# Kernel tuning notes

Hardware: AMD Instinct MI355X
Metric: run time of the kernel (lower is better)

Reference implementation:

```python
import jax, jax.numpy as jnp
import numpy as np

B, S, D = 2, 2048, 1024
H, DK, DV = 16, 64, 64
DF = 4096
EPS = 1e-5


def _layer_norm(x, g, b):
    mu = jnp.mean(x, axis=-1, keepdims=True)
    var = jnp.mean((x - mu) ** 2, axis=-1, keepdims=True)
    return (x - mu) * jax.lax.rsqrt(var + EPS) * g + b


def setup_inputs() -> dict:
    key = jax.random.key(0)
    ks = jax.random.split(key, 12)
    s = lambda fan_in: 1.0 / np.sqrt(fan_in)
    return {
        "enc_input": jax.random.normal(ks[0], (B, S, D), dtype=jnp.float32),
        "wq": jax.random.uniform(ks[1], (D, H * DK), jnp.float32, -s(D), s(D)),
        "wk": jax.random.uniform(ks[2], (D, H * DK), jnp.float32, -s(D), s(D)),
        "wv": jax.random.uniform(ks[3], (D, H * DV), jnp.float32, -s(D), s(D)),
        "wo": jax.random.uniform(ks[4], (H * DV, D), jnp.float32, -s(H * DV), s(H * DV)),
        "w1": jax.random.uniform(ks[5], (D, DF), jnp.float32, -s(D), s(D)),
        "b1": jax.random.uniform(ks[6], (DF,), jnp.float32, -s(D), s(D)),
        "w2": jax.random.uniform(ks[7], (DF, D), jnp.float32, -s(DF), s(DF)),
        "b2": jax.random.uniform(ks[8], (D,), jnp.float32, -s(DF), s(DF)),
        "ln1_g": jnp.ones((D,), jnp.float32),
        "ln1_b": jnp.zeros((D,), jnp.float32),
        "ln2_g": jnp.ones((D,), jnp.float32),
        "ln2_b": jnp.zeros((D,), jnp.float32),
    }


def reference(enc_input, wq, wk, wv, wo, w1, b1, w2, b2, ln1_g, ln1_b, ln2_g, ln2_b):
    x = enc_input
    # QKV projections -> [B, H, S, d]
    q = (x @ wq).reshape(B, S, H, DK).transpose(0, 2, 1, 3)
    k = (x @ wk).reshape(B, S, H, DK).transpose(0, 2, 1, 3)
    v = (x @ wv).reshape(B, S, H, DV).transpose(0, 2, 1, 3)
    # scaled dot-product attention (scale = 1/sqrt(d_k), dropout is identity at eval)
    score = jnp.einsum("bhqd,bhkd->bhqk", q, k) / jnp.sqrt(jnp.float32(DK))
    attn = jax.nn.softmax(score, axis=-1)
    ctx = jnp.einsum("bhqk,bhkd->bhqd", attn, v)
    ctx = ctx.transpose(0, 2, 1, 3).reshape(B, S, H * DV)
    atn_out = ctx @ wo
    # Add & Norm 1
    h = _layer_norm(x + atn_out, ln1_g, ln1_b)
    # FFN
    ffn = jax.nn.relu(h @ w1 + b1) @ w2 + b2
    # Add & Norm 2
    return _layer_norm(h + ffn, ln2_g, ln2_b)
```

## Files before the change

kernel.cpp:

```cpp
#include <hip/hip_runtime.h>
#include <hip/hip_bf16.h>

typedef __bf16 bf16;
typedef __bf16 bf16x4 __attribute__((ext_vector_type(4)));
typedef __bf16 bf16x8 __attribute__((ext_vector_type(8)));
typedef float  f32x4  __attribute__((ext_vector_type(4)));

#define KB 2
#define KS 2048
#define KD 1024
#define KH 16
#define KM (KB*KS)
#define KQKVN 3072
#define KDF 4096

__device__ __forceinline__ f32x4 mfma16(bf16x8 a, bf16x8 b, f32x4 c) {
  return __builtin_amdgcn_mfma_f32_16x16x32_bf16(a, b, c, 0, 0, 0);
}

__device__ __forceinline__ float exp2_hw(float x) {
  float r;
  asm("v_exp_f32 %0, %1" : "=v"(r) : "v"(x));
  return r;
}

__device__ __forceinline__ void g2l16(const bf16* g, bf16* l) {
  __builtin_amdgcn_global_load_lds(
      (const __attribute__((address_space(1))) unsigned int*)g,
      (__attribute__((address_space(3))) unsigned int*)l, 16, 0, 0);
}

__global__ __launch_bounds__(256) void cvt_bf16_kernel(const float* __restrict__ in,
                                                       bf16* __restrict__ out, int n) {
  int i = (blockIdx.x * 256 + threadIdx.x) * 4;
  if (i >= n) return;
  f32x4 v = *reinterpret_cast<const f32x4*>(in + i);
  bf16x4 o;
  o[0] = (bf16)v[0]; o[1] = (bf16)v[1]; o[2] = (bf16)v[2]; o[3] = (bf16)v[3];
  *reinterpret_cast<bf16x4*>(out + i) = o;
}

struct WT4 { const float* src[4]; bf16* dst[4]; };

__global__ __launch_bounds__(256) void wtrans4_kernel(WT4 jobs) {
  __shared__ float tile[32][33];
  const float* W = jobs.src[blockIdx.z];
  bf16* WT = jobs.dst[blockIdx.z];
  const int n0 = blockIdx.x * 32, k0 = blockIdx.y * 32;
  const int tx = threadIdx.x & 31, ty = threadIdx.x >> 5;
#pragma unroll
  for (int j = ty; j < 32; j += 8) tile[j][tx] = W[(size_t)(k0 + j) * 1024 + n0 + tx];
  __syncthreads();
#pragma unroll
  for (int j = ty; j < 32; j += 8)
    WT[(size_t)(n0 + j) * 1024 + k0 + tx] = (bf16)tile[tx][j];
}

__global__ __launch_bounds__(256) void wtrans_big_kernel(const float* __restrict__ w1,
                                                         bf16* __restrict__ w1T,
                                                         const float* __restrict__ w2,
                                                         bf16* __restrict__ w2T) {
  __shared__ float tile[32][33];
  const float* W; bf16* WT; int K, N, n0, k0;
  if (blockIdx.z == 0) {
    W = w1; WT = w1T; K = 1024; N = 4096;
    n0 = blockIdx.x * 32; k0 = blockIdx.y * 32;
  } else {
    W = w2; WT = w2T; K = 4096; N = 1024;
    n0 = blockIdx.y * 32; k0 = blockIdx.x * 32;
  }
  const int tx = threadIdx.x & 31, ty = threadIdx.x >> 5;
#pragma unroll
  for (int j = ty; j < 32; j += 8) tile[j][tx] = W[(size_t)(k0 + j) * N + n0 + tx];
  __syncthreads();
#pragma unroll
  for (int j = ty; j < 32; j += 8) WT[(size_t)(n0 + j) * K + k0 + tx] = (bf16)tile[tx][j];
}

__global__ __launch_bounds__(256) void kvpack_kernel(const bf16* __restrict__ qkv,
                                                     bf16* __restrict__ kp,
                                                     bf16* __restrict__ vt) {
  __shared__ bf16 tile[64][72];
  const int s0 = blockIdx.x * 64;
  const int bh = blockIdx.y;
  const int b = bh >> 4, h = bh & 15;
  const int t = threadIdx.x;
  const int r = t >> 3, c8 = (t & 7) * 8;
#pragma unroll
  for (int rr = r; rr < 64; rr += 32) {
    const size_t grow = (size_t)(b * KS + s0 + rr) * KQKVN + h * 64 + c8;
    bf16x8 kv = *reinterpret_cast<const bf16x8*>(&qkv[grow + 1024]);
    *reinterpret_cast<bf16x8*>(&kp[((size_t)bh * KS + s0 + rr) * 64 + c8]) = kv;
    bf16x8 vv = *reinterpret_cast<const bf16x8*>(&qkv[grow + 2048]);
#pragma unroll
    for (int j = 0; j < 8; j++) tile[rr][c8 + j] = vv[j];
  }
  __syncthreads();
#pragma unroll
  for (int dd = r; dd < 64; dd += 32) {
    bf16x8 v;
#pragma unroll
    for (int j = 0; j < 8; j++) {
      const int pi = c8 + j;
      const int key = ((pi >> 5) << 5) | (((pi >> 2) & 1) << 4) |
                      (((pi >> 3) & 3) << 2) | (pi & 3);
      v[j] = tile[key][dd];
    }
    *reinterpret_cast<bf16x8*>(&vt[(size_t)bh * 64 * KS + (size_t)dd * KS + s0 + c8]) = v;
  }
}

struct P4 { bf16* p[4]; };

template <typename OUT_T, bool RELU, bool HAS_BIAS, bool SPLITK>
__global__ __launch_bounds__(512, 2) void gemm8p(const bf16* __restrict__ A,
                                                 const bf16* __restrict__ BT,
                                                 OUT_T* __restrict__ C, P4 pr,
                                                 const float* __restrict__ bias,
                                                 int M, int N, int K, int Kslice) {
  extern __shared__ __align__(16) bf16 sm[];
  const int tid = threadIdx.x, lane = tid & 63, w = tid >> 6;
  const int wr = w >> 2, wc = w & 3;
  const int gx = gridDim.x;
  const int nwg = gx * gridDim.y;
  int flat = blockIdx.y * gx + blockIdx.x;
  flat = (flat & 7) * (nwg >> 3) + (flat >> 3);
  const int bn = (flat % gx) * 256;
  const int bm = (flat / gx) * 256;
  const int z = blockIdx.z;
  const int NT = (SPLITK ? Kslice : K) >> 6;
  const int lr = lane & 15, hi = lane >> 4;
  const int sqrow = tid >> 3;
  const int sslot = tid & 7;
  const bf16* Abase = A + (size_t)bm * K + (SPLITK ? z * Kslice : 0);
  const bf16* Bbase = BT + (size_t)bn * K + (SPLITK ? z * Kslice : 0);
  auto stageQ = [&](int t, int p) {
    const int row = p * 64 + sqrow;
    const int col = (sslot ^ (row & 7)) * 8;
    bf16* dst = sm + (size_t)(t & 1) * 32768 + p * 4096 + w * 512;
    g2l16(Abase + (size_t)row * K + t * 64 + col, dst);
    g2l16(Bbase + (size_t)row * K + t * 64 + col, dst + 16384);
  };
  f32x4 acc[8][4] = {};
  stageQ(0, 0); stageQ(0, 1); stageQ(0, 2); stageQ(0, 3);
  for (int t = 0; t < NT; t++) {
    const char* sa = (const char*)(sm + (size_t)(t & 1) * 32768);
    const char* sb = sa + 32768;
    bf16x8 af[4], bfr[4];
    if (t + 1 < NT) {
      stageQ(t + 1, 0);
      stageQ(t + 1, 1);
      asm volatile("s_waitcnt vmcnt(4)" ::: "memory");
    } else {
      asm volatile("s_waitcnt vmcnt(0)" ::: "memory");
    }
    __builtin_amdgcn_sched_barrier(0);
    __builtin_amdgcn_s_barrier();
    __builtin_amdgcn_sched_barrier(0);
#pragma unroll
    for (int mfp = 0; mfp < 4; mfp++) {
      const int row = wr * 128 + mfp * 16 + lr;
      af[mfp] = *(const bf16x8*)(sa + row * 128 + ((hi ^ (row & 7)) * 16));
    }
#pragma unroll
    for (int nf = 0; nf < 4; nf++) {
      const int row = wc * 64 + nf * 16 + lr;
      bfr[nf] = *(const bf16x8*)(sb + row * 128 + ((hi ^ (row & 7)) * 16));
    }
    asm volatile("s_waitcnt lgkmcnt(0)" ::: "memory");
    __builtin_amdgcn_sched_barrier(0);
    __builtin_amdgcn_s_setprio(1);
#pragma unroll
    for (int mfp = 0; mfp < 4; mfp++)
#pragma unroll
      for (int nf = 0; nf < 4; nf++)
        acc[mfp][nf] = mfma16(af[mfp], bfr[nf], acc[mfp][nf]);
    __builtin_amdgcn_s_setprio(0);
    if (t + 1 < NT) { stageQ(t + 1, 2); stageQ(t + 1, 3); }
#pragma unroll
    for (int mfp = 0; mfp < 4; mfp++) {
      const int row = wr * 128 + 64 + mfp * 16 + lr;
      af[mfp] = *(const bf16x8*)(sa + row * 128 + ((hi ^ (row & 7)) * 16));
    }
    __builtin_amdgcn_sched_barrier(0);
    __builtin_amdgcn_s_barrier();
    __builtin_amdgcn_sched_barrier(0);
    asm volatile("s_waitcnt lgkmcnt(0)" ::: "memory");
    __builtin_amdgcn_sched_barrier(0);
    __builtin_amdgcn_s_setprio(1);
#pragma unroll
    for (int mfp = 0; mfp < 4; mfp++)
#pragma unroll
      for (int nf = 0; nf < 4; nf++)
        acc[4 + mfp][nf] = mfma16(af[mfp], bfr[nf], acc[4 + mfp][nf]);
    __builtin_amdgcn_s_setprio(0);
#pragma unroll
    for (int mfp = 0; mfp < 4; mfp++) {
      const int row = wr * 128 + mfp * 16 + lr;
      af[mfp] = *(const bf16x8*)(sa + row * 128 + (((4 + hi) ^ (row & 7)) * 16));
    }
#pragma unroll
    for (int nf = 0; nf < 4; nf++) {
      const int row = wc * 64 + nf * 16 + lr;
      bfr[nf] = *(const bf16x8*)(sb + row * 128 + (((4 + hi) ^ (row & 7)) * 16));
    }
    __builtin_amdgcn_sched_barrier(0);
    __builtin_amdgcn_s_barrier();
    __builtin_amdgcn_sched_barrier(0);
    asm volatile("s_waitcnt lgkmcnt(0)" ::: "memory");
    __builtin_amdgcn_sched_barrier(0);
    __builtin_amdgcn_s_setprio(1);
#pragma unroll
    for (int mfp = 0; mfp < 4; mfp++)
#pragma unroll
      for (int nf = 0; nf < 4; nf++)
        acc[mfp][nf] = mfma16(af[mfp], bfr[nf], acc[mfp][nf]);
    __builtin_amdgcn_s_setprio(0);
#pragma unroll
    for (int mfp = 0; mfp < 4; mfp++) {
      const int row = wr * 128 + 64 + mfp * 16 + lr;
      af[mfp] = *(const bf16x8*)(sa + row * 128 + (((4 + hi) ^ (row & 7)) * 16));
    }
    __builtin_amdgcn_sched_barrier(0);
    __builtin_amdgcn_s_barrier();
    __builtin_amdgcn_sched_barrier(0);
    asm volatile("s_waitcnt lgkmcnt(0)" ::: "memory");
    __builtin_amdgcn_sched_barrier(0);
    __builtin_amdgcn_s_setprio(1);
#pragma unroll
    for (int mfp = 0; mfp < 4; mfp++)
#pragma unroll
      for (int nf = 0; nf < 4; nf++)
        acc[4 + mfp][nf] = mfma16(af[mfp], bfr[nf], acc[4 + mfp][nf]);
    __builtin_amdgcn_s_setprio(0);
    __builtin_amdgcn_sched_barrier(0);
    __builtin_amdgcn_s_barrier();
    __builtin_amdgcn_sched_barrier(0);
  }
  const int rg = hi * 4, cl = lr;
  if (SPLITK) {
    bf16* P = pr.p[z];
#pragma unroll
    for (int mf = 0; mf < 8; mf++)
#pragma unroll
      for (int nf = 0; nf < 4; nf++) {
        const int col = bn + wc * 64 + nf * 16 + cl;
#pragma unroll
        for (int i = 0; i < 4; i++) {
          const int row = bm + wr * 128 + mf * 16 + rg + i;
          P[(size_t)row * N + col] = (bf16)acc[mf][nf][i];
        }
      }
  } else {
#pragma unroll
    for (int mf = 0; mf < 8; mf++)
#pragma unroll
      for (int nf = 0; nf < 4; nf++) {
        const int col = bn + wc * 64 + nf * 16 + cl;
        float bv = 0.f;
        if (HAS_BIAS) bv = bias[col];
#pragma unroll
        for (int i = 0; i < 4; i++) {
          const int row = bm + wr * 128 + mf * 16 + rg + i;
          float v = acc[mf][nf][i] + bv;
          if (RELU) v = fmaxf(v, 0.f);
          C[(size_t)row * N + col] = (OUT_T)v;
        }
      }
  }
}

template <typename OUT_T, bool RELU, bool HAS_BIAS, int BN>
__global__ __launch_bounds__(256) void gemm_bt(const bf16* __restrict__ A,
                                               const bf16* __restrict__ BT,
                                               OUT_T* __restrict__ C,
                                               const float* __restrict__ bias,
                                               int M, int N, int K) {
  constexpr int NF = BN / 32;
  __shared__ __align__(16) bf16 sa[2][128 * 32];
  __shared__ __align__(16) bf16 sb[2][BN * 32];
  const int t = threadIdx.x, lane = t & 63, w = t >> 6;
  const int gx = gridDim.x;
  const int nwg = gx * gridDim.y;
  int flat = blockIdx.y * gx + blockIdx.x;
  if ((nwg & 7) == 0) flat = (flat & 7) * (nwg >> 3) + (flat >> 3);
  const int bn = (flat % gx) * BN;
  const int bm = (flat / gx) * 128;
  const int wr = w >> 1, wc = w & 1;
  const int wcol = wc * (BN / 2);
  const int lr = lane & 15, lk = (lane >> 4) * 8;
  const int srow = w * 16 + (lane >> 2);
  const int scol = (lane & 3) * 8;
  f32x4 acc[4][NF] = {};
  const int NT = K >> 5;
  auto stage = [&](int kt, int buf) {
#pragma unroll
    for (int i = 0; i < 2; i++)
      g2l16(A + (size_t)(bm + i * 64 + srow) * K + kt * 32 + scol,
            &sa[buf][(i * 64 + w * 16) * 32]);
#pragma unroll
    for (int i = 0; i < BN / 64; i++)
      g2l16(BT + (size_t)(bn + i * 64 + srow) * K + kt * 32 + scol,
            &sb[buf][(i * 64 + w * 16) * 32]);
  };
  stage(0, 0);
  int cur = 0;
  for (int kt = 0; kt < NT; kt++) {
    __syncthreads();
    if (kt + 1 < NT) stage(kt + 1, cur ^ 1);
    bf16x8 af[4], bfr[NF];
#pragma unroll
    for (int m = 0; m < 4; m++)
      af[m] = *(const bf16x8*)&sa[cur][(wr * 64 + m * 16 + lr) * 32 + lk];
#pragma unroll
    for (int n = 0; n < NF; n++)
      bfr[n] = *(const bf16x8*)&sb[cur][(wcol + n * 16 + lr) * 32 + lk];
#pragma unroll
    for (int m = 0; m < 4; m++)
#pragma unroll
      for (int n = 0; n < NF; n++)
        acc[m][n] = mfma16(af[m], bfr[n], acc[m][n]);
    cur ^= 1;
  }
  const int rg = (lane >> 4) * 4, cl = lane & 15;
#pragma unroll
  for (int m = 0; m < 4; m++)
#pragma unroll
    for (int n = 0; n < NF; n++) {
      const int col = bn + wcol + n * 16 + cl;
      float bv = 0.f;
      if (HAS_BIAS) bv = bias[col];
#pragma unroll
      for (int i = 0; i < 4; i++) {
        const int row = bm + wr * 64 + m * 16 + rg + i;
        float v = acc[m][n][i] + bv;
        if (RELU) v = fmaxf(v, 0.f);
        C[(size_t)row * N + col] = (OUT_T)v;
      }
    }
}

__global__ __launch_bounds__(256) void attn_kernel(const bf16* __restrict__ qkv,
                                                   const bf16* __restrict__ kp,
                                                   const bf16* __restrict__ vt,
                                                   bf16* __restrict__ ctx) {
  __shared__ __align__(16) bf16 ksm[4][64 * 64];
  __shared__ __align__(16) bf16 vsm[4][64 * 64];
  const int t = threadIdx.x, lane = t & 63, w = t >> 6;
  const int flat = blockIdx.y * 16 + blockIdx.x;
  const int xcd = flat & 7, jj = flat >> 3;
  const int bh = xcd + 8 * (jj >> 4);
  const int qb = jj & 15;
  const int b = bh >> 4, h = bh & 15;
  const int qbase = qb * 128 + w * 32;
  const int lr = lane & 15, hi = lane >> 4;
  const int lk = hi * 8, rg = hi * 4, cl = lr;

  bf16x8 aq[2][2];
#pragma unroll
  for (int m = 0; m < 2; m++)
#pragma unroll
    for (int kk = 0; kk < 2; kk++) {
      bf16x8 v = *reinterpret_cast<const bf16x8*>(
          &qkv[(size_t)(b * KS + qbase + m * 16 + lr) * KQKVN + h * 64 + kk * 32 + lk]);
#pragma unroll
      for (int e = 0; e < 8; e++) v[e] = (bf16)((float)v[e] * 0.18033688f);
      aq[m][kk] = v;
    }
  bf16x8 ones;
#pragma unroll
  for (int j = 0; j < 8; j++) ones[j] = (bf16)1.0f;

  const bf16* kpb = kp + (size_t)bh * KS * 64;
  const bf16* vtb = vt + (size_t)bh * 64 * KS;

  auto stageKV = [&](int tt) {
    const int kt0 = tt * 64;
    bf16* kd = &ksm[tt & 3][0];
    bf16* vd = &vsm[tt & 3][0];
#pragma unroll
    for (int i = 0; i < 2; i++) {
      const int q = i * 4096 + w * 1024 + (lane << 4);
      const int row = q >> 7;
      const int slot = ((q >> 4) & 7) ^ (row & 7);
      g2l16(kpb + (size_t)(kt0 + row) * 64 + slot * 8, kd + ((i * 4096 + w * 1024) >> 1));
      g2l16(vtb + (size_t)row * KS + kt0 + slot * 8,   vd + ((i * 4096 + w * 1024) >> 1));
    }
  };

  f32x4 accd[2][4] = {};
  f32x4 lsumv[2] = {};

  stageKV(0); stageKV(1); stageKV(2);
  const int NT = KS / 64;
  for (int tt = 0; tt < NT; tt++) {
    const int rem = NT - 1 - tt;
    if (rem >= 2)      asm volatile("s_waitcnt vmcnt(8)" ::: "memory");
    else if (rem == 1) asm volatile("s_waitcnt vmcnt(4)" ::: "memory");
    else               asm volatile("s_waitcnt vmcnt(0)" ::: "memory");
    __builtin_amdgcn_sched_barrier(0);
    __builtin_amdgcn_s_barrier();
    __builtin_amdgcn_sched_barrier(0);
    if (tt + 3 < NT) stageKV(tt + 3);
    const char* kb = (const char*)&ksm[tt & 3][0];
    const char* vb = (const char*)&vsm[tt & 3][0];
    bf16x8 bk[4][2];
#pragma unroll
    for (int n = 0; n < 4; n++)
#pragma unroll
      for (int kk = 0; kk < 2; kk++) {
        const int row = n * 16 + lr;
        bk[n][kk] = *(const bf16x8*)(kb + row * 128 +
                                     ((kk * 64 + hi * 16) ^ ((row & 7) << 4)));
      }
    f32x4 sc[2][4] = {};
    __builtin_amdgcn_s_setprio(1);
#pragma unroll
    for (int m = 0; m < 2; m++)
#pragma unroll
      for (int n = 0; n < 4; n++)
#pragma unroll
        for (int kk = 0; kk < 2; kk++)
          sc[m][n] = mfma16(bk[n][kk], aq[m][kk], sc[m][n]);
    __builtin_amdgcn_s_setprio(0);
    bf16x8 pa[2][2];
#pragma unroll
    for (int m = 0; m < 2; m++) {
      float p[4][4];
#pragma unroll
      for (int n = 0; n < 4; n++)
#pragma unroll
        for (int i = 0; i < 4; i++)
          p[n][i] = exp2_hw(sc[m][n][i]);
#pragma unroll
      for (int kk = 0; kk < 2; kk++) {
        bf16x8 v;
#pragma unroll
        for (int j = 0; j < 8; j++) v[j] = (bf16)p[kk * 2 + (j >> 2)][j & 3];
        pa[m][kk] = v;
      }
    }
    bf16x8 bv[4][2];
#pragma unroll
    for (int dt = 0; dt < 4; dt++)
#pragma unroll
      for (int kk = 0; kk < 2; kk++) {
        const int row = dt * 16 + lr;
        bv[dt][kk] = *(const bf16x8*)(vb + row * 128 +
                                      ((kk * 64 + hi * 16) ^ ((row & 7) << 4)));
      }
    __builtin_amdgcn_s_setprio(1);
#pragma unroll
    for (int m = 0; m < 2; m++) {
#pragma unroll
      for (int dt = 0; dt < 4; dt++)
#pragma unroll
        for (int kk = 0; kk < 2; kk++)
          accd[m][dt] = mfma16(pa[m][kk], bv[dt][kk], accd[m][dt]);
      lsumv[m] = mfma16(pa[m][0], ones, lsumv[m]);
      lsumv[m] = mfma16(pa[m][1], ones, lsumv[m]);
    }
    __builtin_amdgcn_s_setprio(0);
  }
#pragma unroll
  for (int m = 0; m < 2; m++)
#pragma unroll
    for (int dt = 0; dt < 4; dt++)
#pragma unroll
      for (int i = 0; i < 4; i++)
        ctx[(size_t)(b * KS + qbase + m * 16 + rg + i) * KD + h * 64 + dt * 16 + cl] =
            (bf16)(accd[m][dt][i] / lsumv[m][i]);
}

template <bool ABF, bool OBF>
__global__ __launch_bounds__(256) void ln_kernel(const void* __restrict__ aptr,
                                                 const float* __restrict__ bsum,
                                                 const float* __restrict__ g,
                                                 const float* __restrict__ bet,
                                                 void* __restrict__ outp) {
  const int row = blockIdx.x;
  const int t = threadIdx.x;
  const int lane = t & 63, wid = t >> 6;
  float v[4];
  {
    f32x4 bv = *reinterpret_cast<const f32x4*>(&bsum[(size_t)row * KD + t * 4]);
    if (ABF) {
      bf16x4 av = *reinterpret_cast<const bf16x4*>(
          (const bf16*)aptr + (size_t)row * KD + t * 4);
#pragma unroll
      for (int j = 0; j < 4; j++) v[j] = (float)av[j] + bv[j];
    } else {
      f32x4 av = *reinterpret_cast<const f32x4*>(
          (const float*)aptr + (size_t)row * KD + t * 4);
#pragma unroll
      for (int j = 0; j < 4; j++) v[j] = av[j] + bv[j];
    }
  }
  float s = 0.f, s2 = 0.f;
#pragma unroll
  for (int j = 0; j < 4; j++) { s += v[j]; s2 += v[j] * v[j]; }
#pragma unroll
  for (int off = 32; off; off >>= 1) {
    s += __shfl_xor(s, off, 64);
    s2 += __shfl_xor(s2, off, 64);
  }
  __shared__ float red[8];
  if (lane == 0) { red[wid] = s; red[wid + 4] = s2; }
  __syncthreads();
  s = red[0] + red[1] + red[2] + red[3];
  s2 = red[4] + red[5] + red[6] + red[7];
  const float mu = s * (1.f / KD);
  const float var = s2 * (1.f / KD) - mu * mu;
  const float rs = rsqrtf(var + 1e-5f);
  if (OBF) {
    bf16x4 o;
#pragma unroll
    for (int j = 0; j < 4; j++)
      o[j] = (bf16)((v[j] - mu) * rs * g[t * 4 + j] + bet[t * 4 + j]);
    *reinterpret_cast<bf16x4*>((bf16*)outp + (size_t)row * KD + t * 4) = o;
  } else {
    f32x4 o;
#pragma unroll
    for (int j = 0; j < 4; j++)
      o[j] = (v[j] - mu) * rs * g[t * 4 + j] + bet[t * 4 + j];
    *reinterpret_cast<f32x4*>((float*)outp + (size_t)row * KD + t * 4) = o;
  }
}

__global__ __launch_bounds__(256) void ln2_fused_kernel(const bf16* __restrict__ hh,
                                                        const bf16* __restrict__ p0,
                                                        const bf16* __restrict__ p1,
                                                        const bf16* __restrict__ p2,
                                                        const bf16* __restrict__ p3,
                                                        const float* __restrict__ b2,
                                                        const float* __restrict__ g,
                                                        const float* __restrict__ bet,
                                                        float* __restrict__ outp) {
  const int row = blockIdx.x;
  const int t = threadIdx.x;
  const int lane = t & 63, wid = t >> 6;
  const size_t base = (size_t)row * KD + t * 4;
  bf16x4 hv = *(const bf16x4*)(hh + base);
  bf16x4 a0 = *(const bf16x4*)(p0 + base);
  bf16x4 a1 = *(const bf16x4*)(p1 + base);
  bf16x4 a2 = *(const bf16x4*)(p2 + base);
  bf16x4 a3 = *(const bf16x4*)(p3 + base);
  f32x4 bv = *(const f32x4*)(b2 + t * 4);
  float v[4];
#pragma unroll
  for (int j = 0; j < 4; j++)
    v[j] = (float)hv[j] + (float)a0[j] + (float)a1[j] + (float)a2[j] + (float)a3[j] + bv[j];
  float s = 0.f, s2 = 0.f;
#pragma unroll
  for (int j = 0; j < 4; j++) { s += v[j]; s2 += v[j] * v[j]; }
#pragma unroll
  for (int off = 32; off; off >>= 1) {
    s += __shfl_xor(s, off, 64);
    s2 += __shfl_xor(s2, off, 64);
  }
  __shared__ float red[8];
  if (lane == 0) { red[wid] = s; red[wid + 4] = s2; }
  __syncthreads();
  s = red[0] + red[1] + red[2] + red[3];
  s2 = red[4] + red[5] + red[6] + red[7];
  const float mu = s * (1.f / KD);
  const float var = s2 * (1.f / KD) - mu * mu;
  const float rs = rsqrtf(var + 1e-5f);
  f32x4 o;
#pragma unroll
  for (int j = 0; j < 4; j++)
    o[j] = (v[j] - mu) * rs * g[t * 4 + j] + bet[t * 4 + j];
  *reinterpret_cast<f32x4*>(outp + base) = o;
}

extern "C" void kernel_launch(void* const* d_in, const int* in_sizes, int n_in,
                              void* d_out, int out_size, void* d_ws, size_t ws_size,
                              hipStream_t stream) {
  const float* x     = (const float*)d_in[0];
  const float* wq    = (const float*)d_in[1];
  const float* wk    = (const float*)d_in[2];
  const float* wv    = (const float*)d_in[3];
  const float* wo    = (const float*)d_in[4];
  const float* w1    = (const float*)d_in[5];
  const float* b1    = (const float*)d_in[6];
  const float* w2    = (const float*)d_in[7];
  const float* b2    = (const float*)d_in[8];
  const float* ln1g  = (const float*)d_in[9];
  const float* ln1b  = (const float*)d_in[10];
  const float* ln2g  = (const float*)d_in[11];
  const float* ln2b  = (const float*)d_in[12];
  float* out = (float*)d_out;

  char* ws = (char*)d_ws;
  bf16*  x_bf   = (bf16*)(ws + 0);
  bf16*  wqkvT  = (bf16*)(ws + 8388608);
  bf16*  woT    = (bf16*)(ws + 14680064);
  bf16*  w1T    = (bf16*)(ws + 16777216);
  bf16*  w2T    = (bf16*)(ws + 25165824);
  bf16*  qkv    = (bf16*)(ws + 33554432);
  bf16*  kp     = (bf16*)(ws + 58720256);
  bf16*  vt     = (bf16*)(ws + 67108864);
  float* proj   = (float*)(ws + 75497472);
  bf16*  ctx    = x_bf;
  bf16*  h_bf   = (bf16*)(ws + 8388608);
  bf16*  ffn1   = qkv;
  P4 pr;
  pr.p[0] = (bf16*)(ws + 0);
  pr.p[1] = (bf16*)(ws + 16777216);
  pr.p[2] = (bf16*)(ws + 67108864);
  pr.p[3] = (bf16*)(ws + 75497472);
  P4 pzero = {};

  cvt_bf16_kernel<<<dim3(KM * KD / 1024), 256, 0, stream>>>(x, x_bf, KM * KD);
  WT4 jobs;
  jobs.src[0] = wq; jobs.src[1] = wk; jobs.src[2] = wv; jobs.src[3] = wo;
  jobs.dst[0] = wqkvT;
  jobs.dst[1] = wqkvT + 1024 * 1024;
  jobs.dst[2] = wqkvT + 2048 * 1024;
  jobs.dst[3] = woT;
  wtrans4_kernel<<<dim3(32, 32, 4), 256, 0, stream>>>(jobs);
  wtrans_big_kernel<<<dim3(128, 32, 2), 256, 0, stream>>>(w1, w1T, w2, w2T);

  gemm8p<bf16, false, false, false>
      <<<dim3(KQKVN / 256, KM / 256, 1), 512, 131072, stream>>>(
      x_bf, wqkvT, qkv, pzero, nullptr, KM, KQKVN, KD, KD);

  kvpack_kernel<<<dim3(KS / 64, KB * KH), 256, 0, stream>>>(qkv, kp, vt);

  attn_kernel<<<dim3(KS / 128, KB * KH), 256, 0, stream>>>(qkv, kp, vt, ctx);

  gemm_bt<float, false, false, 64><<<dim3(KD / 64, KM / 128), 256, 0, stream>>>(
      ctx, woT, proj, nullptr, KM, KD, KD);

  ln_kernel<false, true><<<dim3(KM), 256, 0, stream>>>(x, proj, ln1g, ln1b, h_bf);

  gemm8p<bf16, true, true, false>
      <<<dim3(KDF / 256, KM / 256, 1), 512, 131072, stream>>>(
      h_bf, w1T, ffn1, pzero, b1, KM, KDF, KD, KD);

  gemm8p<bf16, false, false, true>
      <<<dim3(KD / 256, KM / 256, 4), 512, 131072, stream>>>(
      ffn1, w2T, (bf16*)nullptr, pr, nullptr, KM, KD, KDF, KDF / 4);

  ln2_fused_kernel<<<dim3(KM), 256, 0, stream>>>(
      h_bf, pr.p[0], pr.p[1], pr.p[2], pr.p[3], b2, ln2g, ln2b, out);
}
```

Measured before the change: 221.5 us.

## Software-pipeline QK^T one tile ahead in attention and drop GEMM sub-step barriers

In the attention kernel, the QK^T MFMA for the next key tile is computed while exp/softmax of the current tile is in progress. The aim is to overlap matrix-core work with the transcendental VALU work, at the cost of extra score registers and a restructured wait/barrier schedule. In the GEMM main loop, the second half of the next-tile prefetch is issued right after the barrier. The three intra-iteration s_barrier plus lgkmcnt waits are removed, leaving the compiler to insert LDS waits, which cuts sync overhead but changes the interleaving.

```diff
diff --git a/kernel.cpp b/kernel.cpp
--- a/kernel.cpp
+++ b/kernel.cpp
@@ -146,7 +146,6 @@
   for (int t = 0; t < NT; t++) {
     const char* sa = (const char*)(sm + (size_t)(t & 1) * 32768);
     const char* sb = sa + 32768;
-    bf16x8 af[4], bfr[4];
     if (t + 1 < NT) {
       stageQ(t + 1, 0);
       stageQ(t + 1, 1);
@@ -157,6 +156,8 @@
     __builtin_amdgcn_sched_barrier(0);
     __builtin_amdgcn_s_barrier();
     __builtin_amdgcn_sched_barrier(0);
+    if (t + 1 < NT) { stageQ(t + 1, 2); stageQ(t + 1, 3); }
+    bf16x8 af[4], bfr[4];
 #pragma unroll
     for (int mfp = 0; mfp < 4; mfp++) {
       const int row = wr * 128 + mfp * 16 + lr;
@@ -167,8 +168,6 @@
       const int row = wc * 64 + nf * 16 + lr;
       bfr[nf] = *(const bf16x8*)(sb + row * 128 + ((hi ^ (row & 7)) * 16));
     }
-    asm volatile("s_waitcnt lgkmcnt(0)" ::: "memory");
-    __builtin_amdgcn_sched_barrier(0);
     __builtin_amdgcn_s_setprio(1);
 #pragma unroll
     for (int mfp = 0; mfp < 4; mfp++)
@@ -176,17 +175,11 @@
       for (int nf = 0; nf < 4; nf++)
         acc[mfp][nf] = mfma16(af[mfp], bfr[nf], acc[mfp][nf]);
     __builtin_amdgcn_s_setprio(0);
-    if (t + 1 < NT) { stageQ(t + 1, 2); stageQ(t + 1, 3); }
 #pragma unroll
     for (int mfp = 0; mfp < 4; mfp++) {
       const int row = wr * 128 + 64 + mfp * 16 + lr;
       af[mfp] = *(const bf16x8*)(sa + row * 128 + ((hi ^ (row & 7)) * 16));
     }
-    __builtin_amdgcn_sched_barrier(0);
-    __builtin_amdgcn_s_barrier();
-    __builtin_amdgcn_sched_barrier(0);
-    asm volatile("s_waitcnt lgkmcnt(0)" ::: "memory");
-    __builtin_amdgcn_sched_barrier(0);
     __builtin_amdgcn_s_setprio(1);
 #pragma unroll
     for (int mfp = 0; mfp < 4; mfp++)
@@ -204,11 +197,6 @@
       const int row = wc * 64 + nf * 16 + lr;
       bfr[nf] = *(const bf16x8*)(sb + row * 128 + (((4 + hi) ^ (row & 7)) * 16));
     }
-    __builtin_amdgcn_sched_barrier(0);
-    __builtin_amdgcn_s_barrier();
-    __builtin_amdgcn_sched_barrier(0);
-    asm volatile("s_waitcnt lgkmcnt(0)" ::: "memory");
-    __builtin_amdgcn_sched_barrier(0);
     __builtin_amdgcn_s_setprio(1);
 #pragma unroll
     for (int mfp = 0; mfp < 4; mfp++)
@@ -221,11 +209,6 @@
       const int row = wr * 128 + 64 + mfp * 16 + lr;
       af[mfp] = *(const bf16x8*)(sa + row * 128 + (((4 + hi) ^ (row & 7)) * 16));
     }
-    __builtin_amdgcn_sched_barrier(0);
-    __builtin_amdgcn_s_barrier();
-    __builtin_amdgcn_sched_barrier(0);
-    asm volatile("s_waitcnt lgkmcnt(0)" ::: "memory");
-    __builtin_amdgcn_sched_barrier(0);
     __builtin_amdgcn_s_setprio(1);
 #pragma unroll
     for (int mfp = 0; mfp < 4; mfp++)
@@ -390,20 +373,21 @@
 
   f32x4 accd[2][4] = {};
   f32x4 lsumv[2] = {};
+  f32x4 sc[2][4];
+#pragma unroll
+  for (int m = 0; m < 2; m++)
+#pragma unroll
+    for (int n = 0; n < 4; n++)
+#pragma unroll
+      for (int e = 0; e < 4; e++) sc[m][n][e] = 0.f;
 
   stageKV(0); stageKV(1); stageKV(2);
-  const int NT = KS / 64;
-  for (int tt = 0; tt < NT; tt++) {
-    const int rem = NT - 1 - tt;
-    if (rem >= 2)      asm volatile("s_waitcnt vmcnt(8)" ::: "memory");
-    else if (rem == 1) asm volatile("s_waitcnt vmcnt(4)" ::: "memory");
-    else               asm volatile("s_waitcnt vmcnt(0)" ::: "memory");
-    __builtin_amdgcn_sched_barrier(0);
-    __builtin_amdgcn_s_barrier();
-    __builtin_amdgcn_sched_barrier(0);
-    if (tt + 3 < NT) stageKV(tt + 3);
-    const char* kb = (const char*)&ksm[tt & 3][0];
-    const char* vb = (const char*)&vsm[tt & 3][0];
+  asm volatile("s_waitcnt vmcnt(8)" ::: "memory");
+  __builtin_amdgcn_sched_barrier(0);
+  __builtin_amdgcn_s_barrier();
+  __builtin_amdgcn_sched_barrier(0);
+  {
+    const char* kb = (const char*)&ksm[0][0];
     bf16x8 bk[4][2];
 #pragma unroll
     for (int n = 0; n < 4; n++)
@@ -413,7 +397,6 @@
         bk[n][kk] = *(const bf16x8*)(kb + row * 128 +
                                      ((kk * 64 + hi * 16) ^ ((row & 7) << 4)));
       }
-    f32x4 sc[2][4] = {};
     __builtin_amdgcn_s_setprio(1);
 #pragma unroll
     for (int m = 0; m < 2; m++)
@@ -423,6 +406,17 @@
         for (int kk = 0; kk < 2; kk++)
           sc[m][n] = mfma16(bk[n][kk], aq[m][kk], sc[m][n]);
     __builtin_amdgcn_s_setprio(0);
+  }
+  const int NT = KS / 64;
+  for (int tt = 0; tt < NT; tt++) {
+    if (tt + 1 < NT) {
+      if (tt + 2 < NT) asm volatile("s_waitcnt vmcnt(4)" ::: "memory");
+      else             asm volatile("s_waitcnt vmcnt(0)" ::: "memory");
+      __builtin_amdgcn_sched_barrier(0);
+      __builtin_amdgcn_s_barrier();
+      __builtin_amdgcn_sched_barrier(0);
+      if (tt + 3 < NT) stageKV(tt + 3);
+    }
     bf16x8 pa[2][2];
 #pragma unroll
     for (int m = 0; m < 2; m++) {
@@ -440,6 +434,34 @@
         pa[m][kk] = v;
       }
     }
+    if (tt + 1 < NT) {
+      const char* kb = (const char*)&ksm[(tt + 1) & 3][0];
+      bf16x8 bk[4][2];
+#pragma unroll
+      for (int n = 0; n < 4; n++)
+#pragma unroll
+        for (int kk = 0; kk < 2; kk++) {
+          const int row = n * 16 + lr;
+          bk[n][kk] = *(const bf16x8*)(kb + row * 128 +
+                                       ((kk * 64 + hi * 16) ^ ((row & 7) << 4)));
+        }
+      f32x4 scn[2][4];
+#pragma unroll
+      for (int m = 0; m < 2; m++)
+#pragma unroll
+        for (int n = 0; n < 4; n++) {
+#pragma unroll
+          for (int e = 0; e < 4; e++) scn[m][n][e] = 0.f;
+#pragma unroll
+          for (int kk = 0; kk < 2; kk++)
+            scn[m][n] = mfma16(bk[n][kk], aq[m][kk], scn[m][n]);
+        }
+#pragma unroll
+      for (int m = 0; m < 2; m++)
+#pragma unroll
+        for (int n = 0; n < 4; n++) sc[m][n] = scn[m][n];
+    }
+    const char* vb = (const char*)&vsm[tt & 3][0];
     bf16x8 bv[4][2];
 #pragma unroll
     for (int dt = 0; dt < 4; dt++)
```

Result: no change. 222.2 us (+0.3%).
